# Kernel optimization log

Measured on AMD Instinct MI355X. Metric: run time of the kernel, lower is better.

The kernel has to match this reference:

```python
import jax, jax.numpy as jnp
import numpy as np

N, E, F, EF, T, C = 50000, 500000, 8, 4, 12, 32


def setup_inputs() -> dict:
    key = jax.random.key(0)
    ks = jax.random.split(key, 16)
    g = lambda i, shape, s=0.2: jax.random.normal(ks[i], shape, jnp.float32) * s
    return {
        "x": jax.random.normal(ks[0], (N, F, T), jnp.float32),
        "edge_index": jax.random.randint(ks[1], (2, E), 0, N),
        "edge_features": jax.random.normal(ks[2], (E, EF), jnp.float32),
        # feature_linear (F -> F)
        "feat_W": g(3, (F, F)), "feat_b": jnp.zeros((F,), jnp.float32),
        # edge_features_linear (EF -> 1)
        "ef_W": g(4, (EF, 1)), "ef_b": jnp.zeros((1,), jnp.float32),
        # A3TGCN attention over periods
        "attention": jax.random.uniform(ks[5], (T,), jnp.float32),
        # TGCN GCNConv weights (F -> C), bias included (PyG default)
        "conv_z_W": g(6, (F, C)), "conv_z_b": jnp.zeros((C,), jnp.float32),
        "conv_r_W": g(7, (F, C)), "conv_r_b": jnp.zeros((C,), jnp.float32),
        "conv_h_W": g(8, (F, C)), "conv_h_b": jnp.zeros((C,), jnp.float32),
        # TGCN gate linears (2C -> C)
        "lin_z_W": g(9, (2 * C, C)), "lin_z_b": jnp.zeros((C,), jnp.float32),
        "lin_r_W": g(10, (2 * C, C)), "lin_r_b": jnp.zeros((C,), jnp.float32),
        "lin_h_W": g(11, (2 * C, C)), "lin_h_b": jnp.zeros((C,), jnp.float32),
        # output head (C -> T)
        "head_W": g(12, (C, T)), "head_b": jnp.zeros((T,), jnp.float32),
    }


def _gcn_norm(edge_index, edge_weight, num_nodes):
    """PyG gcn_norm with add_self_loops=True (fill 1), flow source_to_target."""
    loops = jnp.arange(num_nodes)
    row = jnp.concatenate([edge_index[0], loops])  # sources
    col = jnp.concatenate([edge_index[1], loops])  # targets
    w = jnp.concatenate([edge_weight, jnp.ones((num_nodes,), edge_weight.dtype)])
    deg = jax.ops.segment_sum(w, col, num_segments=num_nodes)
    dinv = jnp.where(deg > 0, jax.lax.rsqrt(jnp.maximum(deg, 1e-12)), 0.0)
    norm = dinv[row] * w * dinv[col]
    return row, col, norm


def _forward(x, edge_index, edge_features, feat_W, feat_b, ef_W, ef_b,
             attention, conv_z_W, conv_z_b, conv_r_W, conv_r_b, conv_h_W,
             conv_h_b, lin_z_W, lin_z_b, lin_r_W, lin_r_b, lin_h_W, lin_h_b,
             head_W, head_b):
    num_nodes = x.shape[0]
    # feature linear over F: [N,F,T] -> [T,N,F]
    xt = jnp.transpose(x, (2, 0, 1)) @ feat_W + feat_b  # [T,N,F]
    # edge weight MLP: [E,EF] -> [E], relu
    ew = jax.nn.relu((edge_features @ ef_W + ef_b)[:, 0])
    row, col, norm = _gcn_norm(edge_index, ew, num_nodes)

    def gcn(h, W, b):
        msg = (h @ W)[row] * norm[:, None]  # [E+N, C]
        return jax.ops.segment_sum(msg, col, num_segments=num_nodes) + b

    def tgcn_cell(x_t):
        # A3TGCN passes H=None each period -> H starts at zeros every period
        H = jnp.zeros((num_nodes, C), x_t.dtype)
        Z = jax.nn.sigmoid(
            jnp.concatenate([gcn(x_t, conv_z_W, conv_z_b), H], 1) @ lin_z_W + lin_z_b)
        R = jax.nn.sigmoid(
            jnp.concatenate([gcn(x_t, conv_r_W, conv_r_b), H], 1) @ lin_r_W + lin_r_b)
        H_tilde = jnp.tanh(
            jnp.concatenate([gcn(x_t, conv_h_W, conv_h_b), H * R], 1) @ lin_h_W + lin_h_b)
        return Z * H + (1.0 - Z) * H_tilde

    probs = jax.nn.softmax(attention)

    def step(acc, inputs):
        x_t, p = inputs
        return acc + p * tgcn_cell(x_t), None

    H_accum, _ = jax.lax.scan(step, jnp.zeros((num_nodes, C), x.dtype), (xt, probs))
    h = jax.nn.relu(H_accum)
    return h @ head_W + head_b  # [N, T]


def reference(x, edge_index, edge_features, feat_W, feat_b, ef_W, ef_b,
              attention, conv_z_W, conv_z_b, conv_r_W, conv_r_b, conv_h_W,
              conv_h_b, lin_z_W, lin_z_b, lin_r_W, lin_r_b, lin_h_W, lin_h_b,
              head_W, head_b):
    return _forward(x, edge_index, edge_features, feat_W, feat_b, ef_W, ef_b,
                    attention, conv_z_W, conv_z_b, conv_r_W, conv_r_b,
                    conv_h_W, conv_h_b, lin_z_W, lin_z_b, lin_r_W, lin_r_b,
                    lin_h_W, lin_h_b, head_W, head_b)
```

## Files before the change

kernel.cpp:

```cpp
#include <hip/hip_runtime.h>
#include <math.h>

#define NN 50000
#define NE 500000
#define FD 8
#define EFD 4
#define TD 12
#define CD 32
#define FT (FD*TD)
#define SLOTS 48
#define ZB 49
#define ZV4 25000
#define L2E 1.4426950408889634f

typedef float f32x2 __attribute__((ext_vector_type(2)));

__global__ __launch_bounds__(512) void kInit(
    float4* __restrict__ zp,
    const float* __restrict__ feat_W, const float* __restrict__ feat_b,
    const float* __restrict__ attention,
    const float* __restrict__ conv_z_W, const float* __restrict__ conv_z_b,
    const float* __restrict__ conv_h_W, const float* __restrict__ conv_h_b,
    const float* __restrict__ lin_z_W, const float* __restrict__ lin_z_b,
    const float* __restrict__ lin_h_W, const float* __restrict__ lin_h_b,
    float* __restrict__ consts)
{
    int tid = threadIdx.x;
    if (blockIdx.x < ZB) {
        int i = blockIdx.x * 512 + tid;
        if (i < ZV4) zp[i] = make_float4(0.f, 0.f, 0.f, 0.f);
        return;
    }
    __shared__ float WL[2][FD*CD];
    int half = tid >> 8;
    int idx  = tid & 255;
    int f = idx >> 5, c = idx & 31;
    float scale = half ? 2.f * L2E : L2E;
    const float* convW = half ? conv_h_W : conv_z_W;
    const float* linW  = half ? lin_h_W  : lin_z_W;
    float acc = 0.f;
    #pragma unroll
    for (int k = 0; k < CD; ++k)
        acc += convW[f*CD + k] * linW[k*CD + c];
    WL[half][idx] = acc;
    __syncthreads();
    float m = 0.f;
    #pragma unroll
    for (int g = 0; g < FD; ++g)
        m += feat_W[f*FD + g] * WL[half][g*CD + c];
    consts[half*256 + idx] = m * scale;
    if (f == 0) {
        float a = 0.f;
        #pragma unroll
        for (int g = 0; g < FD; ++g)
            a += feat_b[g] * WL[half][g*CD + c];
        consts[512 + half*32 + c] = a * scale;
        const float* convB = half ? conv_h_b : conv_z_b;
        const float* linB  = half ? lin_h_b : lin_z_b;
        float cc = linB[c];
        #pragma unroll
        for (int k = 0; k < CD; ++k)
            cc += convB[k] * linW[k*CD + c];
        consts[576 + half*32 + c] = cc * scale;
    }
    if (tid == 0) {
        float mx = attention[0];
        for (int t = 1; t < TD; ++t) mx = fmaxf(mx, attention[t]);
        float e[TD], sum = 0.f;
        for (int t = 0; t < TD; ++t) { e[t] = expf(attention[t] - mx); sum += e[t]; }
        for (int t = 0; t < TD; ++t) consts[640 + t] = e[t] / sum;
    }
}

__global__ void kB1(const int* __restrict__ ei, const float* __restrict__ ef,
                    const float* __restrict__ ef_W, const float* __restrict__ ef_b,
                    unsigned long long* __restrict__ dc, int2* __restrict__ ep)
{
    int e = blockIdx.x * blockDim.x + threadIdx.x;
    if (e >= NE) return;
    float4 f4 = ((const float4*)ef)[e];
    float w = ef_b[0] + f4.x*ef_W[0] + f4.y*ef_W[1] + f4.z*ef_W[2] + f4.w*ef_W[3];
    if (w <= 0.f) return;
    int r = ei[e], c = ei[NE + e];
    unsigned long long pack = (1ULL << 56)
        | (unsigned long long)(w * 4294967296.0f);
    unsigned long long old = atomicAdd(&dc[c], pack);
    int pos = (int)(old >> 56);
    if (pos < SLOTS) ep[c * SLOTS + pos] = make_int2(r, __float_as_int(w));
}

__global__ void kDinv(const unsigned long long* __restrict__ dc,
                      float* __restrict__ dinv, int* __restrict__ cnt,
                      int2* __restrict__ ep)
{
    int n = blockIdx.x * blockDim.x + threadIdx.x;
    if (n >= NN) return;
    unsigned long long v = dc[n];
    float deg = (float)(v & ((1ULL << 56) - 1)) * (1.0f / 4294967296.0f);
    dinv[n] = rsqrtf(deg + 1.0f);
    int m = (int)(v >> 56);
    if (m > SLOTS) m = SLOTS;
    cnt[n] = m;
    int2 pad = make_int2(n, 0);
    for (int i = m; i < 8; ++i) ep[n * SLOTS + i] = pad;
}

__global__ __launch_bounds__(256) void kGE(
    const float* __restrict__ x, const float* __restrict__ dinv,
    const int* __restrict__ cnt, const int2* __restrict__ ep,
    const float* __restrict__ consts, const float* __restrict__ head_W,
    const float* __restrict__ head_b, float* __restrict__ out)
{
    __shared__ float headW[CD*TD];
    __shared__ float ylds[8*FT];
    __shared__ float hlds[8*33];
    int tid = threadIdx.x;
    int c0 = tid & 31;
    int gg = tid >> 5;
    float mzr[FD], mhr[FD];
    #pragma unroll
    for (int f = 0; f < FD; ++f) {
        mzr[f] = consts[f*CD + c0];
        mhr[f] = consts[256 + f*CD + c0];
    }
    float azc = consts[512 + c0], ahc = consts[544 + c0];
    float czc = consts[576 + c0], chc = consts[608 + c0];
    float pt[TD];
    #pragma unroll
    for (int t = 0; t < TD; ++t) pt[t] = consts[640 + t];
    headW[tid] = head_W[tid];
    if (tid < CD*TD - 256) headW[256 + tid] = head_W[256 + tid];
    int base = blockIdx.x * 8;
    int n = base + gg;

    float di = dinv[n];
    float d2 = di * di;
    const float* xrow = x + (size_t)n * FT + c0 * 3;
    float3 xs = *(const float3*)xrow;
    float acc0 = d2*xs.x, acc1 = d2*xs.y, acc2 = d2*xs.z;
    int m = cnt[n];
    int st = n * SLOTS;
    int2 q = ep[st + (c0 & 7)];
    float vvl = __int_as_float(q.y) * dinv[q.x] * di;
    float sv = d2;
    #pragma unroll
    for (int i = 0; i < 8; ++i) {
        int   si = __shfl(q.x, i, 32);
        float vi = __shfl(vvl, i, 32);
        float3 xr = *(const float3*)(x + (size_t)si * FT + c0 * 3);
        acc0 += vi*xr.x; acc1 += vi*xr.y; acc2 += vi*xr.z;
        sv += vi;
    }
    for (int j = st + 8, en = st + m; j < en; ++j) {
        int2 p0 = ep[j];
        float v0 = __int_as_float(p0.y) * dinv[p0.x] * di;
        float3 xr = *(const float3*)(x + (size_t)p0.x * FT + c0 * 3);
        acc0 += v0*xr.x; acc1 += v0*xr.y; acc2 += v0*xr.z;
        sv += v0;
    }
    float* yw = ylds + gg * FT + c0 * 3;
    yw[0] = acc0; yw[1] = acc1; yw[2] = acc2;
    float sn = sv;
    __syncthreads();

    const float4* yf4 = (const float4*)(ylds + gg * FT);
    float bz = czc + sn * azc;
    float bh = chc + sn * ahc;
    f32x2 pz2[6], ph2[6];
    #pragma unroll
    for (int k = 0; k < 6; ++k) {
        pz2[k].x = bz; pz2[k].y = bz;
        ph2[k].x = bh; ph2[k].y = bh;
    }
    #pragma unroll
    for (int f = 0; f < FD; ++f) {
        float4 ya = yf4[f*3 + 0], yb = yf4[f*3 + 1], yc = yf4[f*3 + 2];
        f32x2 y2[6];
        y2[0].x = ya.x; y2[0].y = ya.y;  y2[1].x = ya.z; y2[1].y = ya.w;
        y2[2].x = yb.x; y2[2].y = yb.y;  y2[3].x = yb.z; y2[3].y = yb.w;
        y2[4].x = yc.x; y2[4].y = yc.y;  y2[5].x = yc.z; y2[5].y = yc.w;
        f32x2 mz2, mh2;
        mz2.x = mzr[f]; mz2.y = mzr[f];
        mh2.x = mhr[f]; mh2.y = mhr[f];
        #pragma unroll
        for (int k = 0; k < 6; ++k) {
            asm volatile("v_pk_fma_f32 %0, %1, %2, %0"
                         : "+v"(pz2[k]) : "v"(y2[k]), "v"(mz2));
            asm volatile("v_pk_fma_f32 %0, %1, %2, %0"
                         : "+v"(ph2[k]) : "v"(y2[k]), "v"(mh2));
        }
    }
    float acc = 0.f;
    #pragma unroll
    for (int k = 0; k < 6; ++k) {
        #pragma unroll
        for (int h = 0; h < 2; ++h) {
            float pzv = (h == 0) ? pz2[k].x : pz2[k].y;
            float phv = (h == 0) ? ph2[k].x : ph2[k].y;
            float ez, eh;
            asm("v_exp_f32 %0, %1" : "=v"(ez) : "v"(pzv));
            asm("v_exp_f32 %0, %1" : "=v"(eh) : "v"(phv));
            float omz = __builtin_amdgcn_rcpf(1.f + ez);
            float th  = 1.f - 2.f * __builtin_amdgcn_rcpf(1.f + eh);
            acc += pt[2*k + h] * omz * th;
        }
    }
    hlds[gg*33 + c0] = fmaxf(acc, 0.f);
    __syncthreads();

    if (tid < 8*TD) {
        int n0 = tid / TD, tt = tid - n0*TD;
        float v = head_b[tt];
        const float* hn = hlds + n0*33;
        #pragma unroll
        for (int cc = 0; cc < CD; ++cc) v += hn[cc] * headW[cc*TD + tt];
        out[(size_t)(base + n0)*TD + tt] = v;
    }
}

extern "C" void kernel_launch(void* const* d_in, const int* in_sizes, int n_in,
                              void* d_out, int out_size, void* d_ws, size_t ws_size,
                              hipStream_t stream)
{
    const float* x      = (const float*)d_in[0];
    const int*   ei     = (const int*)  d_in[1];
    const float* ef     = (const float*)d_in[2];
    const float* feat_W = (const float*)d_in[3];
    const float* feat_b = (const float*)d_in[4];
    const float* ef_W   = (const float*)d_in[5];
    const float* ef_b   = (const float*)d_in[6];
    const float* att    = (const float*)d_in[7];
    const float* czW    = (const float*)d_in[8];
    const float* czb    = (const float*)d_in[9];
    const float* chW    = (const float*)d_in[12];
    const float* chb    = (const float*)d_in[13];
    const float* lzW    = (const float*)d_in[14];
    const float* lzb    = (const float*)d_in[15];
    const float* lhW    = (const float*)d_in[18];
    const float* lhb    = (const float*)d_in[19];
    const float* hW     = (const float*)d_in[20];
    const float* hb     = (const float*)d_in[21];
    float* out = (float*)d_out;

    unsigned long long* dc   = (unsigned long long*)d_ws;
    float*              dinv = (float*)(dc + NN);
    int*                cnt  = (int*)(dinv + NN);
    float*              cst  = (float*)(cnt + NN);
    int2*               ep   = (int2*)(cst + 1024);

    kInit<<<ZB + 1, 512, 0, stream>>>((float4*)dc, feat_W, feat_b, att,
                                      czW, czb, chW, chb, lzW, lzb, lhW, lhb, cst);
    kB1<<<(NE + 255)/256, 256, 0, stream>>>(ei, ef, ef_W, ef_b, dc, ep);
    kDinv<<<(NN + 255)/256, 256, 0, stream>>>(dc, dinv, cnt, ep);
    kGE<<<NN/8, 256, 0, stream>>>(x, dinv, cnt, ep, cst, hW, hb, out);
}
```

Baseline: 59.61 us.

## Eliminate kDinv kernel: prefill padding in init, compute dinv on the fly

Removes the separate degree-normalization kernel. The first 8 neighbour slots of every node are now pre-padded with self-index, zero-weight entries in the init kernel, before the scatter kernel runs. The gather kernel decodes degree and count directly from the packed 64-bit counter and recomputes rsqrt for each neighbour. This saves one launch and the dinv/cnt arrays, at the cost of extra 8-byte loads and rsqrt per edge in the gather.

```diff
diff --git a/kernel.cpp b/kernel.cpp
--- a/kernel.cpp
+++ b/kernel.cpp
@@ -11,12 +11,15 @@
 #define SLOTS 48
 #define ZB 49
 #define ZV4 25000
+#define PB 98
 #define L2E 1.4426950408889634f
+#define MASK56 ((1ULL << 56) - 1)
+#define K56 (1.0f / 4294967296.0f)
 
 typedef float f32x2 __attribute__((ext_vector_type(2)));
 
 __global__ __launch_bounds__(512) void kInit(
-    float4* __restrict__ zp,
+    float4* __restrict__ zp, int4* __restrict__ ep4,
     const float* __restrict__ feat_W, const float* __restrict__ feat_b,
     const float* __restrict__ attention,
     const float* __restrict__ conv_z_W, const float* __restrict__ conv_z_b,
@@ -29,6 +32,15 @@
     if (blockIdx.x < ZB) {
         int i = blockIdx.x * 512 + tid;
         if (i < ZV4) zp[i] = make_float4(0.f, 0.f, 0.f, 0.f);
+        return;
+    }
+    if (blockIdx.x < ZB + PB) {
+        int n = (blockIdx.x - ZB) * 512 + tid;
+        if (n < NN) {
+            int4 pad = make_int4(n, 0, n, 0);
+            int4* p = ep4 + n * (SLOTS/2);
+            p[0] = pad; p[1] = pad; p[2] = pad; p[3] = pad;
+        }
         return;
     }
     __shared__ float WL[2][FD*CD];
@@ -89,27 +101,11 @@
     if (pos < SLOTS) ep[c * SLOTS + pos] = make_int2(r, __float_as_int(w));
 }
 
-__global__ void kDinv(const unsigned long long* __restrict__ dc,
-                      float* __restrict__ dinv, int* __restrict__ cnt,
-                      int2* __restrict__ ep)
-{
-    int n = blockIdx.x * blockDim.x + threadIdx.x;
-    if (n >= NN) return;
-    unsigned long long v = dc[n];
-    float deg = (float)(v & ((1ULL << 56) - 1)) * (1.0f / 4294967296.0f);
-    dinv[n] = rsqrtf(deg + 1.0f);
-    int m = (int)(v >> 56);
-    if (m > SLOTS) m = SLOTS;
-    cnt[n] = m;
-    int2 pad = make_int2(n, 0);
-    for (int i = m; i < 8; ++i) ep[n * SLOTS + i] = pad;
-}
-
 __global__ __launch_bounds__(256) void kGE(
-    const float* __restrict__ x, const float* __restrict__ dinv,
-    const int* __restrict__ cnt, const int2* __restrict__ ep,
-    const float* __restrict__ consts, const float* __restrict__ head_W,
-    const float* __restrict__ head_b, float* __restrict__ out)
+    const float* __restrict__ x, const unsigned long long* __restrict__ dc,
+    const int2* __restrict__ ep, const float* __restrict__ consts,
+    const float* __restrict__ head_W, const float* __restrict__ head_b,
+    float* __restrict__ out)
 {
     __shared__ float headW[CD*TD];
     __shared__ float ylds[8*FT];
@@ -133,15 +129,19 @@
     int base = blockIdx.x * 8;
     int n = base + gg;
 
-    float di = dinv[n];
+    unsigned long long vn = dc[n];
+    float di = rsqrtf((float)(vn & MASK56) * K56 + 1.0f);
     float d2 = di * di;
+    int m = (int)(vn >> 56);
+    if (m > SLOTS) m = SLOTS;
     const float* xrow = x + (size_t)n * FT + c0 * 3;
     float3 xs = *(const float3*)xrow;
     float acc0 = d2*xs.x, acc1 = d2*xs.y, acc2 = d2*xs.z;
-    int m = cnt[n];
     int st = n * SLOTS;
     int2 q = ep[st + (c0 & 7)];
-    float vvl = __int_as_float(q.y) * dinv[q.x] * di;
+    unsigned long long sd = dc[q.x];
+    float ds = rsqrtf((float)(sd & MASK56) * K56 + 1.0f);
+    float vvl = __int_as_float(q.y) * ds * di;
     float sv = d2;
     #pragma unroll
     for (int i = 0; i < 8; ++i) {
@@ -153,7 +153,9 @@
     }
     for (int j = st + 8, en = st + m; j < en; ++j) {
         int2 p0 = ep[j];
-        float v0 = __int_as_float(p0.y) * dinv[p0.x] * di;
+        unsigned long long td = dc[p0.x];
+        float tds = rsqrtf((float)(td & MASK56) * K56 + 1.0f);
+        float v0 = __int_as_float(p0.y) * tds * di;
         float3 xr = *(const float3*)(x + (size_t)p0.x * FT + c0 * 3);
         acc0 += v0*xr.x; acc1 += v0*xr.y; acc2 += v0*xr.z;
         sv += v0;
@@ -242,15 +244,13 @@
     const float* hb     = (const float*)d_in[21];
     float* out = (float*)d_out;
 
-    unsigned long long* dc   = (unsigned long long*)d_ws;
-    float*              dinv = (float*)(dc + NN);
-    int*                cnt  = (int*)(dinv + NN);
-    float*              cst  = (float*)(cnt + NN);
-    int2*               ep   = (int2*)(cst + 1024);
-
-    kInit<<<ZB + 1, 512, 0, stream>>>((float4*)dc, feat_W, feat_b, att,
-                                      czW, czb, chW, chb, lzW, lzb, lhW, lhb, cst);
+    unsigned long long* dc  = (unsigned long long*)d_ws;
+    float*              cst = (float*)(dc + NN);
+    int2*               ep  = (int2*)(cst + 1024);
+
+    kInit<<<ZB + PB + 1, 512, 0, stream>>>((float4*)dc, (int4*)ep,
+                                           feat_W, feat_b, att, czW, czb,
+                                           chW, chb, lzW, lzb, lhW, lhb, cst);
     kB1<<<(NE + 255)/256, 256, 0, stream>>>(ei, ef, ef_W, ef_b, dc, ep);
-    kDinv<<<(NN + 255)/256, 256, 0, stream>>>(dc, dinv, cnt, ep);
-    kGE<<<NN/8, 256, 0, stream>>>(x, dinv, cnt, ep, cst, hW, hb, out);
-}
+    kGE<<<NN/8, 256, 0, stream>>>(x, dc, ep, cst, hW, hb, out);
+}
```

After: 57.51 us. -3.5%, faster.
